# Performance work log

Measured on AMD Instinct MI355X. Metric: run time of the kernel, lower is better.

The kernel has to match this reference:

```python
import jax, jax.numpy as jnp
import numpy as np

B, D, K = 8192, 128, 256
RHO = 1.0


def setup_inputs() -> dict:
    key = jax.random.key(0)
    k1, k2, k3 = jax.random.split(key, 3)
    h = jax.random.normal(k1, (B, D), dtype=jnp.float32)
    y = jax.random.randint(k2, (B,), 0, K, dtype=jnp.int64)
    centers = jax.random.normal(k3, (K, D), dtype=jnp.float32)  # nn.Parameter
    return {"h": h, "y": y, "centers": centers}


def reference(h, y, centers):
    # Pairwise squared distances h[b] vs centers[k]: (B, K)
    diff = h[:, None, :] - centers[None, :, :]          # (B, K, D) broadcast
    norm_sq = jnp.sum(diff * diff, axis=2)              # (B, K)
    # Gather distance to the true-class centroid
    distance = jnp.take_along_axis(norm_sq, y[:, None], axis=1)[:, 0]  # (B,)
    # logsumexp over negative euclidean distances
    logsum = jax.nn.logsumexp(-jnp.sqrt(norm_sq), axis=1)              # (B,)
    loss = jnp.mean(distance + logsum)                  # reduction='mean'
    # Regularization: repel nearest centroids (num_classes != 1)
    cdiff = centers[:, None, :] - centers[None, :, :]   # (K, K, D)
    pd = jnp.sum(cdiff * cdiff, axis=2)                 # squared cdist (K, K)
    pd = jnp.where(jnp.eye(K, dtype=bool), jnp.inf, pd)
    reg = jnp.sum(-jnp.min(jnp.log(pd), axis=-1))       # reduction='sum'
    return loss + RHO * reg
```

## Files before the change

kernel.cpp:

```cpp
#include <hip/hip_runtime.h>
#include <math.h>

typedef __attribute__((ext_vector_type(8))) short short8;
typedef __attribute__((ext_vector_type(4))) float f32x4;

constexpr int B = 8192;
constexpr int D = 128;
constexpr int K = 256;
constexpr int RB = K / 16;
constexpr int HB = B / 16;
constexpr int GRID = RB + HB;


__device__ __forceinline__ short8 cvt8(float4 f0, float4 f1, float& sq) {
  sq = fmaf(f0.x, f0.x, fmaf(f0.y, f0.y, fmaf(f0.z, f0.z, fmaf(f0.w, f0.w, sq))));
  sq = fmaf(f1.x, f1.x, fmaf(f1.y, f1.y, fmaf(f1.z, f1.z, fmaf(f1.w, f1.w, sq))));
  union { short8 s; __bf16 b[8]; } u;
  u.b[0] = (__bf16)f0.x; u.b[1] = (__bf16)f0.y;
  u.b[2] = (__bf16)f0.z; u.b[3] = (__bf16)f0.w;
  u.b[4] = (__bf16)f1.x; u.b[5] = (__bf16)f1.y;
  u.b[6] = (__bf16)f1.z; u.b[7] = (__bf16)f1.w;
  return u.s;
}

__global__ __launch_bounds__(256) void cvt_kernel(const float* __restrict__ centers,
                                                  short8* __restrict__ cbu,
                                                  float* __restrict__ cc) {
  const int ci = blockIdx.x;
  const int t = threadIdx.x;
  const int base = ci * 2048 + t * 8;
  const float4* p = reinterpret_cast<const float4*>(centers + base);
  float sq = 0.f;
  short8 o = cvt8(p[0], p[1], sq);
  cbu[ci * 256 + t] = o;
#pragma unroll
  for (int off = 1; off < 16; off <<= 1) sq += __shfl_xor(sq, off);
  if ((t & 15) == 0) cc[base / 128] = sq;
}

__global__ __launch_bounds__(256) void main_kernel(
    const float* __restrict__ h, const int* __restrict__ y,
    const float* __restrict__ centers, const short8* __restrict__ cbu,
    const float* __restrict__ cc,
    float* __restrict__ part_loss, float* __restrict__ part_reg_sum) {
  const int t = threadIdx.x;
  const int w = t >> 6;
  const int l = t & 63;
  const int lr = l & 15;
  const int lg = l >> 4;
  const bool isreg = (blockIdx.x < RB);
  const int r0 = (isreg ? (int)blockIdx.x : (int)blockIdx.x - RB) * 16;
  const float* Ap = (isreg ? centers : h) + (size_t)(r0 + lr) * D + lg * 8;
  const int n0 = w * 64;

  short8 a[4];
  float sq = 0.f;
#pragma unroll
  for (int c = 0; c < 4; ++c) {
    const float4* p = reinterpret_cast<const float4*>(Ap + c * 32);
    a[c] = cvt8(p[0], p[1], sq);
  }
  sq += __shfl_xor(sq, 16);
  sq += __shfl_xor(sq, 32);
  float rr[4];
#pragma unroll
  for (int j = 0; j < 4; ++j)
    rr[j] = __int_as_float(
        __builtin_amdgcn_ds_bpermute((lg * 4 + j) << 2, __float_as_int(sq)));

  f32x4 zero = {0.f, 0.f, 0.f, 0.f};
  f32x4 acc[4] = {zero, zero, zero, zero};
#pragma unroll
  for (int c = 0; c < 4; ++c) {
#pragma unroll
    for (int n = 0; n < 4; ++n) {
      short8 bfrag = cbu[(size_t)(n0 + n * 16 + lr) * (D / 8) + c * 4 + lg];
      acc[n] = __builtin_amdgcn_mfma_f32_16x16x32_bf16(a[c], bfrag, acc[n], 0, 0, 0);
    }
  }

  __shared__ float ls[4][16];
  __shared__ float ldy[4][16];

  if (!isreg) {
    int y_r[4];
#pragma unroll
    for (int j = 0; j < 4; ++j) y_r[j] = y[r0 + lg * 4 + j];
    float s[4] = {0.f, 0.f, 0.f, 0.f}, dyv[4] = {0.f, 0.f, 0.f, 0.f};
#pragma unroll
    for (int n = 0; n < 4; ++n) {
      const int colg = n0 + n * 16 + lr;
      const float ccv = cc[colg];
#pragma unroll
      for (int j = 0; j < 4; ++j) {
        float dist = fmaxf(fmaf(-2.f, acc[n][j], rr[j] + ccv), 0.f);
        if (y_r[j] == colg) dyv[j] = dist;
        s[j] += __expf(-sqrtf(dist));
      }
    }
#pragma unroll
    for (int j = 0; j < 4; ++j) {
#pragma unroll
      for (int off = 1; off < 16; off <<= 1) {
        s[j]   += __shfl_xor(s[j], off);
        dyv[j] += __shfl_xor(dyv[j], off);
      }
    }
    if (lr == 0) {
#pragma unroll
      for (int j = 0; j < 4; ++j) {
        ls[w][lg * 4 + j]  = s[j];
        ldy[w][lg * 4 + j] = dyv[j];
      }
    }
    __syncthreads();
    if (t < 16) {
      float stot = (ls[0][t] + ls[1][t]) + (ls[2][t] + ls[3][t]);
      float dtot = (ldy[0][t] + ldy[1][t]) + (ldy[2][t] + ldy[3][t]);
      float v = dtot + logf(fmaxf(stot, 1e-37f));
#pragma unroll
      for (int off = 1; off < 16; off <<= 1) v += __shfl_xor(v, off);
      if (t == 0) part_loss[blockIdx.x - RB] = v;
    }
  } else {
    float pmin[4] = {INFINITY, INFINITY, INFINITY, INFINITY};
#pragma unroll
    for (int n = 0; n < 4; ++n) {
      const int colg = n0 + n * 16 + lr;
      const float ccv = cc[colg];
#pragma unroll
      for (int j = 0; j < 4; ++j) {
        const int irow = r0 + lg * 4 + j;
        float pd = fmaf(-2.f, acc[n][j], rr[j] + ccv);
        if (colg != irow) pmin[j] = fminf(pmin[j], pd);
      }
    }
#pragma unroll
    for (int j = 0; j < 4; ++j) {
#pragma unroll
      for (int off = 1; off < 16; off <<= 1)
        pmin[j] = fminf(pmin[j], __shfl_xor(pmin[j], off));
    }
    if (lr == 0) {
#pragma unroll
      for (int j = 0; j < 4; ++j) ls[w][lg * 4 + j] = pmin[j];
    }
    __syncthreads();
    if (t < 16) {
      float m = fminf(fminf(ls[0][t], ls[1][t]), fminf(ls[2][t], ls[3][t]));
      float v = -logf(fmaxf(m, 1e-37f));
#pragma unroll
      for (int off = 1; off < 16; off <<= 1) v += __shfl_xor(v, off);
      if (t == 0) part_reg_sum[blockIdx.x] = v;
    }
  }
}

__global__ __launch_bounds__(256) void final_kernel(
    const float* __restrict__ part_loss, const float* __restrict__ part_reg_sum,
    float* __restrict__ out) {
  const int t = threadIdx.x;
  float v = (part_loss[t] + part_loss[t + 256]) * (1.0f / (float)B);
  if (t < RB) v += part_reg_sum[t];
  const int lane = t & 63;
  const int wid  = t >> 6;
#pragma unroll
  for (int off = 32; off; off >>= 1) v += __shfl_xor(v, off);
  __shared__ float red[4];
  if (lane == 0) red[wid] = v;
  __syncthreads();
  if (t == 0) out[0] = red[0] + red[1] + red[2] + red[3];
}

extern "C" void kernel_launch(void* const* d_in, const int* in_sizes, int n_in,
                              void* d_out, int out_size, void* d_ws, size_t ws_size,
                              hipStream_t stream) {
  const float* h       = (const float*)d_in[0];
  const int*   y       = (const int*)d_in[1];
  const float* centers = (const float*)d_in[2];
  float* out = (float*)d_out;
  float* ws  = (float*)d_ws;

  float*  cc           = ws;
  float*  part_reg_sum = ws + 256;
  float*  part_loss    = ws + 512;
  short8* cbu          = reinterpret_cast<short8*>(ws + 1024);

  cvt_kernel<<<16, 256, 0, stream>>>(centers, cbu, cc);
  main_kernel<<<GRID, 256, 0, stream>>>(h, y, centers, cbu, cc, part_loss, part_reg_sum);
  final_kernel<<<1, 256, 0, stream>>>(part_loss, part_reg_sum, out);
}
```

Measured before the change: 22.06 us.

## Move center-repulsion regularizer into prep kernel, reading fp32 centers directly

The regularization blocks (center-vs-center min distance) move from the main kernel into the prep kernel, where they convert fp32 centers to bf16 on the fly instead of waiting for the converted buffer. The main kernel then runs only the uniform h-row blocks, with no per-block branch, and loads y earlier. This shrinks the main grid and removes divergent block types from it. In exchange the prep kernel does more work on its critical path before the main kernel can start.

```diff
diff --git a/kernel.cpp b/kernel.cpp
--- a/kernel.cpp
+++ b/kernel.cpp
@@ -7,9 +7,7 @@
 constexpr int B = 8192;
 constexpr int D = 128;
 constexpr int K = 256;
-constexpr int RB = K / 16;
 constexpr int HB = B / 16;
-constexpr int GRID = RB + HB;
 
 
 __device__ __forceinline__ short8 cvt8(float4 f0, float4 f1, float& sq) {
@@ -23,38 +21,113 @@
   return u.s;
 }
 
-__global__ __launch_bounds__(256) void cvt_kernel(const float* __restrict__ centers,
-                                                  short8* __restrict__ cbu,
-                                                  float* __restrict__ cc) {
-  const int ci = blockIdx.x;
+__global__ __launch_bounds__(256) void prep_kernel(
+    const float* __restrict__ centers, short8* __restrict__ cbu,
+    float* __restrict__ cc, float* __restrict__ part_reg_sum) {
   const int t = threadIdx.x;
-  const int base = ci * 2048 + t * 8;
-  const float4* p = reinterpret_cast<const float4*>(centers + base);
+  if (blockIdx.x < 16) {
+    const int ci = blockIdx.x;
+    const int base = ci * 2048 + t * 8;
+    const float4* p = reinterpret_cast<const float4*>(centers + base);
+    float sq = 0.f;
+    short8 o = cvt8(p[0], p[1], sq);
+    cbu[ci * 256 + t] = o;
+#pragma unroll
+    for (int off = 1; off < 16; off <<= 1) sq += __shfl_xor(sq, off);
+    if ((t & 15) == 0) cc[base / 128] = sq;
+    return;
+  }
+
+  const int w = t >> 6;
+  const int l = t & 63;
+  const int lr = l & 15;
+  const int lg = l >> 4;
+  const int r0 = ((int)blockIdx.x - 16) * 16;
+  const float* Ap = centers + (size_t)(r0 + lr) * D + lg * 8;
+  const int n0 = w * 64;
+
+  short8 a[4];
   float sq = 0.f;
-  short8 o = cvt8(p[0], p[1], sq);
-  cbu[ci * 256 + t] = o;
-#pragma unroll
-  for (int off = 1; off < 16; off <<= 1) sq += __shfl_xor(sq, off);
-  if ((t & 15) == 0) cc[base / 128] = sq;
+#pragma unroll
+  for (int c = 0; c < 4; ++c) {
+    const float4* p = reinterpret_cast<const float4*>(Ap + c * 32);
+    a[c] = cvt8(p[0], p[1], sq);
+  }
+  sq += __shfl_xor(sq, 16);
+  sq += __shfl_xor(sq, 32);
+  float rr[4];
+#pragma unroll
+  for (int j = 0; j < 4; ++j)
+    rr[j] = __int_as_float(
+        __builtin_amdgcn_ds_bpermute((lg * 4 + j) << 2, __float_as_int(sq)));
+
+  f32x4 zero = {0.f, 0.f, 0.f, 0.f};
+  f32x4 acc[4] = {zero, zero, zero, zero};
+  float cs[4] = {0.f, 0.f, 0.f, 0.f};
+#pragma unroll
+  for (int c = 0; c < 4; ++c) {
+#pragma unroll
+    for (int n = 0; n < 4; ++n) {
+      const float4* p = reinterpret_cast<const float4*>(
+          centers + (size_t)(n0 + n * 16 + lr) * D + c * 32 + lg * 8);
+      short8 bfrag = cvt8(p[0], p[1], cs[n]);
+      acc[n] = __builtin_amdgcn_mfma_f32_16x16x32_bf16(a[c], bfrag, acc[n], 0, 0, 0);
+    }
+  }
+#pragma unroll
+  for (int n = 0; n < 4; ++n) {
+    cs[n] += __shfl_xor(cs[n], 16);
+    cs[n] += __shfl_xor(cs[n], 32);
+  }
+
+  float pmin[4] = {INFINITY, INFINITY, INFINITY, INFINITY};
+#pragma unroll
+  for (int n = 0; n < 4; ++n) {
+    const int colg = n0 + n * 16 + lr;
+    const float ccv = cs[n];
+#pragma unroll
+    for (int j = 0; j < 4; ++j) {
+      const int irow = r0 + lg * 4 + j;
+      float pd = fmaf(-2.f, acc[n][j], rr[j] + ccv);
+      if (colg != irow) pmin[j] = fminf(pmin[j], pd);
+    }
+  }
+#pragma unroll
+  for (int j = 0; j < 4; ++j)
+#pragma unroll
+    for (int off = 1; off < 16; off <<= 1)
+      pmin[j] = fminf(pmin[j], __shfl_xor(pmin[j], off));
+
+  __shared__ float ls[4][16];
+  if (lr == 0) {
+#pragma unroll
+    for (int j = 0; j < 4; ++j) ls[w][lg * 4 + j] = pmin[j];
+  }
+  __syncthreads();
+  if (t < 16) {
+    float m = fminf(fminf(ls[0][t], ls[1][t]), fminf(ls[2][t], ls[3][t]));
+    float v = -logf(fmaxf(m, 1e-37f));
+#pragma unroll
+    for (int off = 1; off < 16; off <<= 1) v += __shfl_xor(v, off);
+    if (t == 0) part_reg_sum[blockIdx.x - 16] = v;
+  }
 }
 
 __global__ __launch_bounds__(256) void main_kernel(
     const float* __restrict__ h, const int* __restrict__ y,
-    const float* __restrict__ centers, const short8* __restrict__ cbu,
-    const float* __restrict__ cc,
-    float* __restrict__ part_loss, float* __restrict__ part_reg_sum) {
+    const short8* __restrict__ cbu, const float* __restrict__ cc,
+    float* __restrict__ part_loss) {
   const int t = threadIdx.x;
   const int w = t >> 6;
   const int l = t & 63;
   const int lr = l & 15;
   const int lg = l >> 4;
-  const bool isreg = (blockIdx.x < RB);
-  const int r0 = (isreg ? (int)blockIdx.x : (int)blockIdx.x - RB) * 16;
-  const float* Ap = (isreg ? centers : h) + (size_t)(r0 + lr) * D + lg * 8;
+  const int r0 = blockIdx.x * 16;
   const int n0 = w * 64;
 
   short8 a[4];
   float sq = 0.f;
+  const float* Ap = h + (size_t)(r0 + lr) * D + lg * 8;
 #pragma unroll
   for (int c = 0; c < 4; ++c) {
     const float4* p = reinterpret_cast<const float4*>(Ap + c * 32);
@@ -63,10 +136,13 @@
   sq += __shfl_xor(sq, 16);
   sq += __shfl_xor(sq, 32);
   float rr[4];
-#pragma unroll
-  for (int j = 0; j < 4; ++j)
+  int y_r[4];
+#pragma unroll
+  for (int j = 0; j < 4; ++j) {
     rr[j] = __int_as_float(
         __builtin_amdgcn_ds_bpermute((lg * 4 + j) << 2, __float_as_int(sq)));
+    y_r[j] = y[r0 + lg * 4 + j];
+  }
 
   f32x4 zero = {0.f, 0.f, 0.f, 0.f};
   f32x4 acc[4] = {zero, zero, zero, zero};
@@ -79,80 +155,43 @@
     }
   }
 
+  float s[4] = {0.f, 0.f, 0.f, 0.f}, dyv[4] = {0.f, 0.f, 0.f, 0.f};
+#pragma unroll
+  for (int n = 0; n < 4; ++n) {
+    const int colg = n0 + n * 16 + lr;
+    const float ccv = cc[colg];
+#pragma unroll
+    for (int j = 0; j < 4; ++j) {
+      float dist = fmaxf(fmaf(-2.f, acc[n][j], rr[j] + ccv), 0.f);
+      if (y_r[j] == colg) dyv[j] = dist;
+      s[j] += __expf(-sqrtf(dist));
+    }
+  }
+#pragma unroll
+  for (int j = 0; j < 4; ++j) {
+#pragma unroll
+    for (int off = 1; off < 16; off <<= 1) {
+      s[j]   += __shfl_xor(s[j], off);
+      dyv[j] += __shfl_xor(dyv[j], off);
+    }
+  }
   __shared__ float ls[4][16];
   __shared__ float ldy[4][16];
-
-  if (!isreg) {
-    int y_r[4];
-#pragma unroll
-    for (int j = 0; j < 4; ++j) y_r[j] = y[r0 + lg * 4 + j];
-    float s[4] = {0.f, 0.f, 0.f, 0.f}, dyv[4] = {0.f, 0.f, 0.f, 0.f};
-#pragma unroll
-    for (int n = 0; n < 4; ++n) {
-      const int colg = n0 + n * 16 + lr;
-      const float ccv = cc[colg];
-#pragma unroll
-      for (int j = 0; j < 4; ++j) {
-        float dist = fmaxf(fmaf(-2.f, acc[n][j], rr[j] + ccv), 0.f);
-        if (y_r[j] == colg) dyv[j] = dist;
-        s[j] += __expf(-sqrtf(dist));
-      }
-    }
+  if (lr == 0) {
 #pragma unroll
     for (int j = 0; j < 4; ++j) {
-#pragma unroll
-      for (int off = 1; off < 16; off <<= 1) {
-        s[j]   += __shfl_xor(s[j], off);
-        dyv[j] += __shfl_xor(dyv[j], off);
-      }
-    }
-    if (lr == 0) {
-#pragma unroll
-      for (int j = 0; j < 4; ++j) {
-        ls[w][lg * 4 + j]  = s[j];
-        ldy[w][lg * 4 + j] = dyv[j];
-      }
-    }
-    __syncthreads();
-    if (t < 16) {
-      float stot = (ls[0][t] + ls[1][t]) + (ls[2][t] + ls[3][t]);
-      float dtot = (ldy[0][t] + ldy[1][t]) + (ldy[2][t] + ldy[3][t]);
-      float v = dtot + logf(fmaxf(stot, 1e-37f));
-#pragma unroll
-      for (int off = 1; off < 16; off <<= 1) v += __shfl_xor(v, off);
-      if (t == 0) part_loss[blockIdx.x - RB] = v;
-    }
-  } else {
-    float pmin[4] = {INFINITY, INFINITY, INFINITY, INFINITY};
-#pragma unroll
-    for (int n = 0; n < 4; ++n) {
-      const int colg = n0 + n * 16 + lr;
-      const float ccv = cc[colg];
-#pragma unroll
-      for (int j = 0; j < 4; ++j) {
-        const int irow = r0 + lg * 4 + j;
-        float pd = fmaf(-2.f, acc[n][j], rr[j] + ccv);
-        if (colg != irow) pmin[j] = fminf(pmin[j], pd);
-      }
-    }
-#pragma unroll
-    for (int j = 0; j < 4; ++j) {
-#pragma unroll
-      for (int off = 1; off < 16; off <<= 1)
-        pmin[j] = fminf(pmin[j], __shfl_xor(pmin[j], off));
-    }
-    if (lr == 0) {
-#pragma unroll
-      for (int j = 0; j < 4; ++j) ls[w][lg * 4 + j] = pmin[j];
-    }
-    __syncthreads();
-    if (t < 16) {
-      float m = fminf(fminf(ls[0][t], ls[1][t]), fminf(ls[2][t], ls[3][t]));
-      float v = -logf(fmaxf(m, 1e-37f));
-#pragma unroll
-      for (int off = 1; off < 16; off <<= 1) v += __shfl_xor(v, off);
-      if (t == 0) part_reg_sum[blockIdx.x] = v;
-    }
+      ls[w][lg * 4 + j]  = s[j];
+      ldy[w][lg * 4 + j] = dyv[j];
+    }
+  }
+  __syncthreads();
+  if (t < 16) {
+    float stot = (ls[0][t] + ls[1][t]) + (ls[2][t] + ls[3][t]);
+    float dtot = (ldy[0][t] + ldy[1][t]) + (ldy[2][t] + ldy[3][t]);
+    float v = dtot + logf(fmaxf(stot, 1e-37f));
+#pragma unroll
+    for (int off = 1; off < 16; off <<= 1) v += __shfl_xor(v, off);
+    if (t == 0) part_loss[blockIdx.x] = v;
   }
 }
 
@@ -161,7 +200,7 @@
     float* __restrict__ out) {
   const int t = threadIdx.x;
   float v = (part_loss[t] + part_loss[t + 256]) * (1.0f / (float)B);
-  if (t < RB) v += part_reg_sum[t];
+  if (t < 16) v += part_reg_sum[t];
   const int lane = t & 63;
   const int wid  = t >> 6;
 #pragma unroll
@@ -169,7 +208,7 @@
   __shared__ float red[4];
   if (lane == 0) red[wid] = v;
   __syncthreads();
-  if (t == 0) out[0] = red[0] + red[1] + red[2] + red[3];
+  if (t == 0) out[0] = (red[0] + red[1]) + (red[2] + red[3]);
 }
 
 extern "C" void kernel_launch(void* const* d_in, const int* in_sizes, int n_in,
@@ -186,7 +225,7 @@
   float*  part_loss    = ws + 512;
   short8* cbu          = reinterpret_cast<short8*>(ws + 1024);
 
-  cvt_kernel<<<16, 256, 0, stream>>>(centers, cbu, cc);
-  main_kernel<<<GRID, 256, 0, stream>>>(h, y, centers, cbu, cc, part_loss, part_reg_sum);
+  prep_kernel<<<32, 256, 0, stream>>>(centers, cbu, cc, part_reg_sum);
+  main_kernel<<<HB, 256, 0, stream>>>(h, y, cbu, cc, part_loss);
   final_kernel<<<1, 256, 0, stream>>>(part_loss, part_reg_sum, out);
 }
```

New measurement: 21.82 us. Within noise of the previous version (-1.1%).
